# Optimization experiments

Measured on AMD Instinct MI355X. Metric: run time of the kernel, lower is better.

The kernel has to match this reference:

```python
import jax, jax.numpy as jnp
import numpy as np

N = 50000   # num_of_nodes (cfg.dataset.num_nodes)
C = 128     # in_channels; TopKPooling ratio = C/N -> k = C pooled nodes
E = 800000  # num edges


def setup_inputs() -> dict:
    key = jax.random.key(0)
    ks = jax.random.split(key, 8)
    std = 1.0 / np.sqrt(C)
    X = jax.random.normal(ks[0], (N, C), dtype=jnp.float32)
    edge_index = jax.random.randint(ks[1], (2, E), 0, N, dtype=jnp.int64)
    edge_weight = jax.random.uniform(ks[2], (E,), dtype=jnp.float32)
    p = jax.random.normal(ks[3], (C,), dtype=jnp.float32)                      # TopKPooling projection
    W_ih = jax.random.normal(ks[4], (3 * C, C), dtype=jnp.float32) * std       # GRU input weights [r|z|n]
    W_hh = jax.random.normal(ks[5], (3 * C, C), dtype=jnp.float32) * std       # GRU hidden weights
    b_ih = jnp.zeros((3 * C,), dtype=jnp.float32)
    b_hh = jnp.zeros((3 * C,), dtype=jnp.float32)
    W_conv = jax.random.uniform(ks[6], (C, C), dtype=jnp.float32, minval=-std, maxval=std)  # GCN lin weight
    b_conv = jnp.zeros((C,), dtype=jnp.float32)
    return {"X": X, "edge_weight": edge_weight, "p": p, "W_ih": W_ih, "W_hh": W_hh,
            "b_ih": b_ih, "b_hh": b_hh, "W_conv": W_conv, "b_conv": b_conv,
            "edge_index": edge_index}


def _forward(X, edge_weight, p, W_ih, W_hh, b_ih, b_hh, W_conv, b_conv, edge_index):
    # ---- TopKPooling: score = X.p/||p||, pick top k=C nodes, gate with tanh ----
    score = X @ p / jnp.linalg.norm(p)                       # [N]
    top_vals, top_idx = jax.lax.top_k(score, C)              # k = C (ratio = C/N)
    X_tilde = X[top_idx] * jnp.tanh(top_vals)[:, None]       # [C, C]
    X_tilde = jax.lax.stop_gradient(X_tilde)                 # .detach() in original

    # ---- GRU single step: input X_tilde (batch=C), hidden h0 = W_conv ----
    gi = X_tilde @ W_ih.T + b_ih                             # [C, 3C]
    gh = W_conv @ W_hh.T + b_hh                              # [C, 3C]
    gi_r, gi_z, gi_n = jnp.split(gi, 3, axis=-1)
    gh_r, gh_z, gh_n = jnp.split(gh, 3, axis=-1)
    r = jax.nn.sigmoid(gi_r + gh_r)
    z = jax.nn.sigmoid(gi_z + gh_z)
    n = jnp.tanh(gi_n + r * gh_n)
    W_new = (1.0 - z) * n + z * W_conv                       # evolved GCN weight [C, C]

    # ---- GCNConv with self-loops + symmetric normalization ----
    src, dst = edge_index[0], edge_index[1]
    loop = jnp.arange(N, dtype=src.dtype)
    src2 = jnp.concatenate([src, loop])
    dst2 = jnp.concatenate([dst, loop])
    w2 = jnp.concatenate([edge_weight, jnp.ones((N,), dtype=edge_weight.dtype)])
    deg = jax.ops.segment_sum(w2, dst2, num_segments=N)      # [N]
    dinv = jnp.where(deg > 0, jax.lax.rsqrt(deg), 0.0)
    norm = dinv[src2] * w2 * dinv[dst2]                      # [E+N]
    Xw = X @ W_new.T                                         # [N, C]
    msg = Xw[src2] * norm[:, None]                           # gather + scale, [E+N, C]
    out = jax.ops.segment_sum(msg, dst2, num_segments=N)     # scatter-add, [N, C]
    return out + b_conv


def reference(X, edge_weight, p, W_ih, W_hh, b_ih, b_hh, W_conv, b_conv, edge_index):
    return _forward(X, edge_weight, p, W_ih, W_hh, b_ih, b_hh, W_conv, b_conv, edge_index)
```

## Files before the change

kernel.cpp:

```cpp
#include <hip/hip_runtime.h>
#include <hip/hip_fp16.h>
#include <math.h>

#define C 128
#define HB 2048
#define NS 4096
#define SHB 192

typedef __attribute__((ext_vector_type(8))) short bf16x8;
typedef __attribute__((ext_vector_type(4))) float f32x4;

__device__ inline unsigned ord_f32(float f) {
    unsigned u = __float_as_uint(f);
    return u ^ ((u & 0x80000000u) ? 0xFFFFFFFFu : 0x80000000u);
}
__device__ inline float unord_f32(unsigned u) {
    return __uint_as_float(u ^ ((u & 0x80000000u) ? 0x80000000u : 0xFFFFFFFFu));
}
__device__ inline short f2bf(float f) {
    unsigned u = __float_as_uint(f);
    return (short)((u + 0x7FFFu + ((u >> 16) & 1u)) >> 16);
}
__device__ inline float bf2f(short s) {
    return __uint_as_float(((unsigned)(unsigned short)s) << 16);
}

__global__ __launch_bounds__(1024) void k_front(const float* __restrict__ X,
                                                const float* __restrict__ p,
                                                float* __restrict__ scores,
                                                int* __restrict__ hist,
                                                const int* __restrict__ ei,
                                                int* __restrict__ rh,
                                                int N, int E, int NBIN, int NBLKE) {
    int t = threadIdx.x;
    if (blockIdx.x < SHB) {
        __shared__ int lh[HB];
        for (int i = t; i < HB; i += 1024) lh[i] = 0;
        __syncthreads();
        int gw   = blockIdx.x * 16 + (t >> 6);
        int lane = t & 63;
        const float2* p2 = (const float2*)p;
        float2 pv2 = p2[lane];
        for (int r = gw; r < N; r += SHB * 16) {
            const float2* xr = (const float2*)(X + (size_t)r * C);
            float2 x2 = xr[lane];
            float a = x2.x * pv2.x + x2.y * pv2.y;
            #pragma unroll
            for (int o = 32; o; o >>= 1) a += __shfl_down(a, o);
            if (lane == 0) {
                scores[r] = a;
                atomicAdd(&lh[ord_f32(a) >> 21], 1);
            }
        }
        __syncthreads();
        for (int i = t; i < HB; i += 1024) {
            int v = lh[i];
            if (v) atomicAdd(&hist[i], v);
        }
    } else {
        __shared__ int bh[8][256];
        int cp = (t >> 7) & 7;
        for (int i = t; i < 8 * 256; i += 1024) ((int*)bh)[i] = 0;
        __syncthreads();
        int eb = blockIdx.x - SHB;
        int e = eb * 2048 + t * 2;
        if (e + 1 < E) {
            int2 d2 = *(const int2*)(ei + E + e);
            atomicAdd(&bh[cp][d2.x >> 8], 1);
            atomicAdd(&bh[cp][d2.y >> 8], 1);
        } else if (e < E) {
            atomicAdd(&bh[cp][ei[E + e] >> 8], 1);
        }
        __syncthreads();
        for (int i = t; i < NBIN; i += 1024) {
            int s = 0;
            #pragma unroll
            for (int c = 0; c < 8; c++) s += bh[c][i];
            rh[(size_t)i * NBLKE + eb] = s;
        }
    }
}

__global__ __launch_bounds__(512) void k_rscanA(int* __restrict__ rh, int* __restrict__ tot, int NBLKE) {
    __shared__ int sc[512];
    int t = threadIdx.x;
    int bin = blockIdx.x;
    int v = (t < NBLKE) ? rh[(size_t)bin * NBLKE + t] : 0;
    sc[t] = v;
    __syncthreads();
    for (int off = 1; off < 512; off <<= 1) {
        int u = (t >= off) ? sc[t - off] : 0;
        __syncthreads();
        sc[t] += u;
        __syncthreads();
    }
    if (t < NBLKE) rh[(size_t)bin * NBLKE + t] = sc[t] - v;
    if (t == 511) tot[bin] = sc[511];
}

__global__ __launch_bounds__(1024) void k_rscat(const int* __restrict__ ei, const float* __restrict__ ew,
                                                const int* __restrict__ rh, const int* __restrict__ tot,
                                                unsigned long long* __restrict__ sorted,
                                                int E, int NBIN, int NBLKE) {
    __shared__ int sc[256];
    __shared__ int cur[256];
    int t = threadIdx.x;
    int eb = blockIdx.x;
    int v = 0;
    if (t < 256) {
        v = (t < NBIN) ? tot[t] : 0;
        sc[t] = v;
    }
    __syncthreads();
    for (int off = 1; off < 256; off <<= 1) {
        int u = (t < 256 && t >= off) ? sc[t - off] : 0;
        __syncthreads();
        if (t < 256) sc[t] += u;
        __syncthreads();
    }
    if (t < NBIN) cur[t] = (sc[t] - v) + rh[(size_t)t * NBLKE + eb];
    __syncthreads();
    int e = eb * 2048 + t * 2;
    #pragma unroll
    for (int j = 0; j < 2; j++) {
        int ee = e + j;
        if (ee < E) {
            int s = ei[ee], d = ei[E + ee];
            float w = ew[ee];
            int pos = atomicAdd(&cur[d >> 8], 1);
            unsigned long long pk = ((unsigned long long)(unsigned)d << 48)
                                  | ((unsigned long long)(unsigned short)s << 32)
                                  |  (unsigned long long)__float_as_uint(w);
            sorted[pos] = pk;
        }
    }
}

__global__ __launch_bounds__(1024) void k_bin(const unsigned long long* __restrict__ sorted,
                                              const int* __restrict__ tot,
                                              int* __restrict__ offs, float* __restrict__ dinv,
                                              unsigned* __restrict__ epack,
                                              int N, int E, int NBIN) {
    __shared__ int cnt[256];
    __shared__ float wsum[256];
    __shared__ int sc[256];
    __shared__ int cur2[256];
    __shared__ int s_base[2];
    int t = threadIdx.x;
    int b = blockIdx.x;
    int v = 0;
    if (t < 256) {
        v = (t < NBIN) ? tot[t] : 0;
        sc[t] = v;
    }
    __syncthreads();
    for (int off = 1; off < 256; off <<= 1) {
        int u = (t < 256 && t >= off) ? sc[t - off] : 0;
        __syncthreads();
        if (t < 256) sc[t] += u;
        __syncthreads();
    }
    if (t == b) { s_base[0] = sc[t] - v; s_base[1] = sc[t]; }
    __syncthreads();
    int s0 = s_base[0], s1 = s_base[1];
    for (int i = t; i < 256; i += 1024) { cnt[i] = 0; wsum[i] = 0.f; }
    __syncthreads();
    for (int i = s0 + t; i < s1; i += 1024) {
        unsigned long long pk = sorted[i];
        int d8 = (int)(pk >> 48) & 255;
        float w = __uint_as_float((unsigned)(pk & 0xFFFFFFFFull));
        atomicAdd(&cnt[d8], 1);
        atomicAdd(&wsum[d8], w);
    }
    __syncthreads();
    int cv = (t < 256) ? cnt[t] : 0;
    if (t < 256) sc[t] = cv;
    __syncthreads();
    for (int off = 1; off < 256; off <<= 1) {
        int u = (t < 256 && t >= off) ? sc[t - off] : 0;
        __syncthreads();
        if (t < 256) sc[t] += u;
        __syncthreads();
    }
    if (t < 256) {
        int loff = sc[t] - cv;
        cur2[t] = s0 + loff;
        int node = b * 256 + t;
        if (node < N) {
            offs[node] = s0 + loff;
            dinv[node] = rsqrtf(1.0f + wsum[t]);
        }
    }
    if (b == NBIN - 1 && t == 0) offs[N] = E;
    __syncthreads();
    for (int i = s0 + t; i < s1; i += 1024) {
        unsigned long long pk = sorted[i];
        int d8 = (int)(pk >> 48) & 255;
        unsigned src = (unsigned)((pk >> 32) & 0xFFFFu);
        float w = __uint_as_float((unsigned)(pk & 0xFFFFFFFFull));
        int pos = atomicAdd(&cur2[d8], 1);
        __half hw = __float2half(w);
        epack[pos] = ((unsigned)*(unsigned short*)&hw << 16) | src;
    }
}

__global__ __launch_bounds__(256) void k_filter(const float* __restrict__ scores,
                                                const int* __restrict__ hist,
                                                int* __restrict__ nc,
                                                unsigned long long* __restrict__ cand, int N) {
    __shared__ int sc[256];
    __shared__ int sT;
    int t = threadIdx.x;
    int loc[8];
    int sum = 0;
    #pragma unroll
    for (int s = 0; s < 8; s++) {
        loc[s] = hist[HB - 1 - (t * 8 + s)];
        sum += loc[s];
    }
    sc[t] = sum;
    __syncthreads();
    for (int off = 1; off < 256; off <<= 1) {
        int v = (t >= off) ? sc[t - off] : 0;
        __syncthreads();
        sc[t] += v;
        __syncthreads();
    }
    int run = sc[t] - sum;
    #pragma unroll
    for (int s = 0; s < 8; s++) {
        int b = HB - 1 - (t * 8 + s);
        int nr = run + loc[s];
        if (run < C && nr >= C) sT = b;
        run = nr;
    }
    __syncthreads();
    int T = sT;
    int i = blockIdx.x * 256 + t;
    if (i < N) {
        unsigned u = ord_f32(scores[i]);
        if ((int)(u >> 21) >= T) {
            int pos = atomicAdd(nc, 1);
            if (pos < NS)
                cand[pos] = ((unsigned long long)u << 32) | (unsigned)(~(unsigned)i);
        }
    }
}

__global__ __launch_bounds__(1024) void k_sel(const unsigned long long* __restrict__ cand,
                                              const int* __restrict__ nc,
                                              const float* __restrict__ p,
                                              int* __restrict__ tidx, float* __restrict__ gate) {
    __shared__ unsigned long long sk[NS];
    __shared__ float red[16];
    __shared__ float s_pn;
    int t = threadIdx.x;
    int M = *nc; if (M > NS) M = NS;
    int S = 256; while (S < M) S <<= 1;
    for (int i = t; i < S; i += 1024) sk[i] = (i < M) ? cand[i] : 0ULL;
    float pv = 0.f;
    if (t < C) { float x = p[t]; pv = x * x; }
    #pragma unroll
    for (int o = 32; o; o >>= 1) pv += __shfl_down(pv, o);
    if ((t & 63) == 0) red[t >> 6] = pv;
    __syncthreads();
    if (t == 0) {
        float s = 0.f;
        for (int i = 0; i < 16; i++) s += red[i];
        s_pn = sqrtf(s);
    }
    for (int k = 2; k <= S; k <<= 1) {
        for (int j = k >> 1; j > 0; j >>= 1) {
            __syncthreads();
            for (int idx = t; idx < S; idx += 1024) {
                int l = idx ^ j;
                if (l > idx) {
                    unsigned long long a = sk[idx], b = sk[l];
                    bool desc = (idx & k) == 0;
                    if (desc ? (a < b) : (a > b)) { sk[idx] = b; sk[l] = a; }
                }
            }
        }
    }
    __syncthreads();
    if (t < C) {
        unsigned long long g = sk[t];
        tidx[t] = (int)(~(unsigned)(g & 0xFFFFFFFFull));
        gate[t] = tanhf(unord_f32((unsigned)(g >> 32)) / s_pn);
    }
}

__global__ __launch_bounds__(256) void k_gru(const float* __restrict__ X,
                                             const int* __restrict__ tidx,
                                             const float* __restrict__ gate,
                                             const float* __restrict__ Wc,
                                             const float* __restrict__ W_ih, const float* __restrict__ W_hh,
                                             const float* __restrict__ b_ih, const float* __restrict__ b_hh,
                                             float* __restrict__ wnewT) {
    int t = threadIdx.x;
    int i = t & 127;
    int j = blockIdx.x * 2 + (t >> 7);
    int src = tidx[i];
    float g = gate[i];
    const float4* xr   = (const float4*)(X + (size_t)src * C);
    const float4* hr   = (const float4*)(Wc + (size_t)i * C);
    const float4* wri  = (const float4*)(W_ih + (size_t)j * C);
    const float4* wzi  = (const float4*)(W_ih + (size_t)(C + j) * C);
    const float4* wni  = (const float4*)(W_ih + (size_t)(2 * C + j) * C);
    const float4* wrh  = (const float4*)(W_hh + (size_t)j * C);
    const float4* wzh  = (const float4*)(W_hh + (size_t)(C + j) * C);
    const float4* wnh  = (const float4*)(W_hh + (size_t)(2 * C + j) * C);
    float gir = 0, giz = 0, gin = 0, ghr = 0, ghz = 0, ghn = 0;
    #pragma unroll 8
    for (int k4 = 0; k4 < C / 4; k4++) {
        float4 x = xr[k4], h = hr[k4], a;
        a = wri[k4]; gir += x.x * a.x + x.y * a.y + x.z * a.z + x.w * a.w;
        a = wzi[k4]; giz += x.x * a.x + x.y * a.y + x.z * a.z + x.w * a.w;
        a = wni[k4]; gin += x.x * a.x + x.y * a.y + x.z * a.z + x.w * a.w;
        a = wrh[k4]; ghr += h.x * a.x + h.y * a.y + h.z * a.z + h.w * a.w;
        a = wzh[k4]; ghz += h.x * a.x + h.y * a.y + h.z * a.z + h.w * a.w;
        a = wnh[k4]; ghn += h.x * a.x + h.y * a.y + h.z * a.z + h.w * a.w;
    }
    gir = g * gir + b_ih[j];         ghr += b_hh[j];
    giz = g * giz + b_ih[C + j];     ghz += b_hh[C + j];
    gin = g * gin + b_ih[2 * C + j]; ghn += b_hh[2 * C + j];
    float r = 1.f / (1.f + expf(-(gir + ghr)));
    float z = 1.f / (1.f + expf(-(giz + ghz)));
    float n = tanhf(gin + r * ghn);
    float wn = (1.f - z) * n + z * Wc[(size_t)i * C + j];
    wnewT[(size_t)j * C + i] = wn;
}

__global__ __launch_bounds__(256) void k_xw(const float* __restrict__ X,
                                            const float* __restrict__ wnewT,
                                            const float* __restrict__ dinv,
                                            unsigned* __restrict__ xwh, int N) {
    __shared__ short Bh[C * C];
    __shared__ short Bl[C * C];
    int t = threadIdx.x;
    for (int idx = t; idx < C * C; idx += 256) {
        int k = idx >> 7, c = idx & 127;
        float wv = wnewT[idx];
        short hi = f2bf(wv);
        float lo = wv - bf2f(hi);
        int pos = c * C + (k ^ ((c & 15) << 3));
        Bh[pos] = hi;
        Bl[pos] = f2bf(lo);
    }
    __syncthreads();

    int wave = t >> 6, lane = t & 63;
    int ln = lane & 15, quad = lane >> 4;
    int r0 = blockIdx.x * 128 + wave * 32;

    f32x4 acc[2][8];
    #pragma unroll
    for (int mt = 0; mt < 2; mt++)
        #pragma unroll
        for (int ct = 0; ct < 8; ct++) { acc[mt][ct][0] = 0.f; acc[mt][ct][1] = 0.f; acc[mt][ct][2] = 0.f; acc[mt][ct][3] = 0.f; }

    int row0 = r0 + ln;       if (row0 >= N) row0 = N - 1;
    int row1 = r0 + 16 + ln;  if (row1 >= N) row1 = N - 1;
    const float* xr0 = X + (size_t)row0 * C + quad * 8;
    const float* xr1 = X + (size_t)row1 * C + quad * 8;

    for (int ks = 0; ks < 4; ks++) {
        float a0[8], a1[8];
        *(float4*)&a0[0] = *(const float4*)(xr0 + ks * 32);
        *(float4*)&a0[4] = *(const float4*)(xr0 + ks * 32 + 4);
        *(float4*)&a1[0] = *(const float4*)(xr1 + ks * 32);
        *(float4*)&a1[4] = *(const float4*)(xr1 + ks * 32 + 4);
        bf16x8 a0h, a0l, a1h, a1l;
        #pragma unroll
        for (int j = 0; j < 8; j++) {
            short h0 = f2bf(a0[j]); a0h[j] = h0; a0l[j] = f2bf(a0[j] - bf2f(h0));
            short h1 = f2bf(a1[j]); a1h[j] = h1; a1l[j] = f2bf(a1[j] - bf2f(h1));
        }
        int kb = ks * 32 + quad * 8;
        int koff = kb ^ (ln << 3);
        #pragma unroll
        for (int ct = 0; ct < 8; ct++) {
            int pos = (ct * 16 + ln) * C + koff;
            bf16x8 bh = *(bf16x8*)&Bh[pos];
            bf16x8 bl = *(bf16x8*)&Bl[pos];
            acc[0][ct] = __builtin_amdgcn_mfma_f32_16x16x32_bf16(a0h, bh, acc[0][ct], 0, 0, 0);
            acc[0][ct] = __builtin_amdgcn_mfma_f32_16x16x32_bf16(a0l, bh, acc[0][ct], 0, 0, 0);
            acc[0][ct] = __builtin_amdgcn_mfma_f32_16x16x32_bf16(a0h, bl, acc[0][ct], 0, 0, 0);
            acc[1][ct] = __builtin_amdgcn_mfma_f32_16x16x32_bf16(a1h, bh, acc[1][ct], 0, 0, 0);
            acc[1][ct] = __builtin_amdgcn_mfma_f32_16x16x32_bf16(a1l, bh, acc[1][ct], 0, 0, 0);
            acc[1][ct] = __builtin_amdgcn_mfma_f32_16x16x32_bf16(a1h, bl, acc[1][ct], 0, 0, 0);
        }
    }

    __half* H = (__half*)xwh;
    #pragma unroll
    for (int mt = 0; mt < 2; mt++) {
        int rbase = r0 + mt * 16 + quad * 4;
        #pragma unroll
        for (int reg = 0; reg < 4; reg++) {
            int r = rbase + reg;
            if (r < N) {
                float dvr = dinv[r];
                #pragma unroll
                for (int ct = 0; ct < 8; ct++) {
                    int col = ct * 16 + ln;
                    H[(size_t)r * C + col] = __float2half(acc[mt][ct][reg] * dvr);
                }
            }
        }
    }
}

__global__ __launch_bounds__(256) void k_gather(const unsigned* __restrict__ xwh,
                                                const int* __restrict__ offs,
                                                const unsigned* __restrict__ epack,
                                                const float* __restrict__ dinv,
                                                const float* __restrict__ b_conv,
                                                float* __restrict__ out, int N) {
    int t = threadIdx.x;
    int v = blockIdx.x * 4 + (t >> 6);
    int lane = t & 63;
    if (v >= N) return;
    float dv = dinv[v];
    unsigned uv = xwh[(size_t)v * 64 + lane];
    __half2 hv = *(__half2*)&uv;
    float acc0 = __low2float(hv);
    float acc1 = __high2float(hv);
    int e0 = offs[v], e1 = offs[v + 1];
    int e = e0;
    for (; e + 7 < e1; e += 8) {
        unsigned pk[8], ux[8];
        #pragma unroll
        for (int j = 0; j < 8; j++) pk[j] = __builtin_nontemporal_load(&epack[e + j]);
        #pragma unroll
        for (int j = 0; j < 8; j++) ux[j] = xwh[(size_t)(pk[j] & 0xFFFFu) * 64 + lane];
        #pragma unroll
        for (int j = 0; j < 8; j++) {
            unsigned short hs = (unsigned short)(pk[j] >> 16);
            float nm = __half2float(*(__half*)&hs);
            __half2 h = *(__half2*)&ux[j];
            acc0 += nm * __low2float(h);
            acc1 += nm * __high2float(h);
        }
    }
    for (; e + 3 < e1; e += 4) {
        unsigned pk[4], ux[4];
        #pragma unroll
        for (int j = 0; j < 4; j++) pk[j] = __builtin_nontemporal_load(&epack[e + j]);
        #pragma unroll
        for (int j = 0; j < 4; j++) ux[j] = xwh[(size_t)(pk[j] & 0xFFFFu) * 64 + lane];
        #pragma unroll
        for (int j = 0; j < 4; j++) {
            unsigned short hs = (unsigned short)(pk[j] >> 16);
            float nm = __half2float(*(__half*)&hs);
            __half2 h = *(__half2*)&ux[j];
            acc0 += nm * __low2float(h);
            acc1 += nm * __high2float(h);
        }
    }
    for (; e < e1; e++) {
        unsigned pA = __builtin_nontemporal_load(&epack[e]);
        unsigned uA = xwh[(size_t)(pA & 0xFFFFu) * 64 + lane];
        unsigned short hs = (unsigned short)(pA >> 16);
        float nA = __half2float(*(__half*)&hs);
        __half2 hA = *(__half2*)&uA;
        acc0 += nA * __low2float(hA);
        acc1 += nA * __high2float(hA);
    }
    const float2* b2 = (const float2*)b_conv;
    float2 bb = b2[lane];
    unsigned long long ov = ((unsigned long long)__float_as_uint(acc1 * dv + bb.y) << 32)
                          |  (unsigned long long)__float_as_uint(acc0 * dv + bb.x);
    __builtin_nontemporal_store(ov, (unsigned long long*)(out + (size_t)v * C) + lane);
}

extern "C" void kernel_launch(void* const* d_in, const int* in_sizes, int n_in,
                              void* d_out, int out_size, void* d_ws, size_t ws_size,
                              hipStream_t stream) {
    const float* X      = (const float*)d_in[0];
    const float* ew     = (const float*)d_in[1];
    const float* p      = (const float*)d_in[2];
    const float* W_ih   = (const float*)d_in[3];
    const float* W_hh   = (const float*)d_in[4];
    const float* b_ih   = (const float*)d_in[5];
    const float* b_hh   = (const float*)d_in[6];
    const float* W_conv = (const float*)d_in[7];
    const float* b_conv = (const float*)d_in[8];
    const int*   ei     = (const int*)d_in[9];
    const int N = in_sizes[0] / C;
    const int E = in_sizes[1];
    float* out = (float*)d_out;
    const int NB    = (N + 255) / 256;
    const int NBIN  = (N + 255) / 256;
    const int NBLKE = (E + 2047) / 2048;

    char* w = (char*)d_ws;
    auto alloc = [&](size_t bytes) -> void* {
        void* r = (void*)w;
        w += (bytes + 255) & ~(size_t)255;
        return r;
    };
    int*   hist   = (int*)alloc(HB * 4);
    int*   nc     = (int*)alloc(256);
    size_t zbytes = (size_t)(w - (char*)d_ws);
    float* scores = (float*)alloc((size_t)N * 4);
    float* dinv   = (float*)alloc((size_t)N * 4);
    int*   offs   = (int*)alloc((size_t)(N + 1) * 4);
    int*   rh     = (int*)alloc((size_t)NBIN * NBLKE * 4);
    int*   tot    = (int*)alloc((size_t)NBIN * 4);
    unsigned long long* cand = (unsigned long long*)alloc((size_t)NS * 8);
    int*   tidx   = (int*)alloc(C * 4);
    float* gate   = (float*)alloc(C * 4);
    float* wnewT  = (float*)alloc((size_t)C * C * 4);
    unsigned long long* sorted = (unsigned long long*)alloc((size_t)E * 8);
    unsigned* epack = (unsigned*)alloc((size_t)E * 4);
    unsigned* xwh = (unsigned*)alloc((size_t)N * 64 * 4);

    hipMemsetAsync(d_ws, 0, zbytes, stream);
    k_front<<<SHB + NBLKE, 1024, 0, stream>>>(X, p, scores, hist, ei, rh, N, E, NBIN, NBLKE);
    k_filter<<<NB, 256, 0, stream>>>(scores, hist, nc, cand, N);
    k_sel<<<1, 1024, 0, stream>>>(cand, nc, p, tidx, gate);
    k_gru<<<C / 2, 256, 0, stream>>>(X, tidx, gate, W_conv, W_ih, W_hh, b_ih, b_hh, wnewT);
    k_rscanA<<<NBIN, 512, 0, stream>>>(rh, tot, NBLKE);
    k_rscat<<<NBLKE, 1024, 0, stream>>>(ei, ew, rh, tot, sorted, E, NBIN, NBLKE);
    k_bin<<<NBIN, 1024, 0, stream>>>(sorted, tot, offs, dinv, epack, N, E, NBIN);
    k_xw<<<(N + 127) / 128, 256, 0, stream>>>(X, wnewT, dinv, xwh, N);
    k_gather<<<(N + 3) / 4, 256, 0, stream>>>(xwh, offs, epack, dinv, b_conv, out, N);
}
```

Before: 225.2 us.

## Fuse top-k filter and select, cache bin edges in LDS, unroll gather by 16

Merges the multi-block candidate filter and the single-block bitonic select into one single-block kernel that scans all scores and collects candidates in shared memory, removing a launch and the global candidate buffer and counter. k_bin now stashes its sorted edge slice in LDS during the counting pass so the second pass reads from LDS instead of global memory. The gather inner loop is unrolled from 8 to 16 edges for more loads in flight. The fused select runs the 50k-score scan on one block, which may be slower than the old parallel filter, and the larger LDS use in k_bin and the deeper unroll may cut occupancy.

```diff
diff --git a/kernel.cpp b/kernel.cpp
--- a/kernel.cpp
+++ b/kernel.cpp
@@ -6,6 +6,7 @@
 #define HB 2048
 #define NS 4096
 #define SHB 192
+#define BCAP 6144
 
 typedef __attribute__((ext_vector_type(8))) short bf16x8;
 typedef __attribute__((ext_vector_type(4))) float f32x4;
@@ -81,6 +82,78 @@
     }
 }
 
+__global__ __launch_bounds__(1024) void k_fsel(const float* __restrict__ scores,
+                                               const int* __restrict__ hist,
+                                               const float* __restrict__ p,
+                                               int* __restrict__ tidx, float* __restrict__ gate,
+                                               int N) {
+    __shared__ unsigned long long sk[NS];
+    __shared__ int hsc[1024];
+    __shared__ int sT;
+    __shared__ int s_nc;
+    __shared__ float red[16];
+    __shared__ float s_pn;
+    int t = threadIdx.x;
+    int b0 = HB - 1 - 2 * t, b1 = HB - 2 - 2 * t;
+    int l0 = hist[b0], l1 = hist[b1];
+    int sum = l0 + l1;
+    hsc[t] = sum;
+    if (t == 0) s_nc = 0;
+    __syncthreads();
+    for (int off = 1; off < 1024; off <<= 1) {
+        int v = (t >= off) ? hsc[t - off] : 0;
+        __syncthreads();
+        hsc[t] += v;
+        __syncthreads();
+    }
+    int run = hsc[t] - sum;
+    if (run < C && run + l0 >= C) sT = b0;
+    if (run + l0 < C && run + l0 + l1 >= C) sT = b1;
+    __syncthreads();
+    int T = sT;
+    for (int i = t; i < N; i += 1024) {
+        unsigned u = ord_f32(scores[i]);
+        if ((int)(u >> 21) >= T) {
+            int pos = atomicAdd(&s_nc, 1);
+            if (pos < NS)
+                sk[pos] = ((unsigned long long)u << 32) | (unsigned)(~(unsigned)i);
+        }
+    }
+    float pv = 0.f;
+    if (t < C) { float x = p[t]; pv = x * x; }
+    #pragma unroll
+    for (int o = 32; o; o >>= 1) pv += __shfl_down(pv, o);
+    if ((t & 63) == 0) red[t >> 6] = pv;
+    __syncthreads();
+    if (t == 0) {
+        float s = 0.f;
+        for (int i = 0; i < 16; i++) s += red[i];
+        s_pn = sqrtf(s);
+    }
+    int M = s_nc; if (M > NS) M = NS;
+    int S = 256; while (S < M) S <<= 1;
+    for (int i = t; i < S; i += 1024) if (i >= M) sk[i] = 0ULL;
+    for (int k = 2; k <= S; k <<= 1) {
+        for (int j = k >> 1; j > 0; j >>= 1) {
+            __syncthreads();
+            for (int idx = t; idx < S; idx += 1024) {
+                int l = idx ^ j;
+                if (l > idx) {
+                    unsigned long long a = sk[idx], b = sk[l];
+                    bool desc = (idx & k) == 0;
+                    if (desc ? (a < b) : (a > b)) { sk[idx] = b; sk[l] = a; }
+                }
+            }
+        }
+    }
+    __syncthreads();
+    if (t < C) {
+        unsigned long long g = sk[t];
+        tidx[t] = (int)(~(unsigned)(g & 0xFFFFFFFFull));
+        gate[t] = tanhf(unord_f32((unsigned)(g >> 32)) / s_pn);
+    }
+}
+
 __global__ __launch_bounds__(512) void k_rscanA(int* __restrict__ rh, int* __restrict__ tot, int NBLKE) {
     __shared__ int sc[512];
     int t = threadIdx.x;
@@ -141,6 +214,7 @@
                                               int* __restrict__ offs, float* __restrict__ dinv,
                                               unsigned* __restrict__ epack,
                                               int N, int E, int NBIN) {
+    __shared__ unsigned long long ebuf[BCAP];
     __shared__ int cnt[256];
     __shared__ float wsum[256];
     __shared__ int sc[256];
@@ -167,6 +241,8 @@
     __syncthreads();
     for (int i = s0 + t; i < s1; i += 1024) {
         unsigned long long pk = sorted[i];
+        int li = i - s0;
+        if (li < BCAP) ebuf[li] = pk;
         int d8 = (int)(pk >> 48) & 255;
         float w = __uint_as_float((unsigned)(pk & 0xFFFFFFFFull));
         atomicAdd(&cnt[d8], 1);
@@ -194,99 +270,14 @@
     if (b == NBIN - 1 && t == 0) offs[N] = E;
     __syncthreads();
     for (int i = s0 + t; i < s1; i += 1024) {
-        unsigned long long pk = sorted[i];
+        int li = i - s0;
+        unsigned long long pk = (li < BCAP) ? ebuf[li] : sorted[i];
         int d8 = (int)(pk >> 48) & 255;
         unsigned src = (unsigned)((pk >> 32) & 0xFFFFu);
         float w = __uint_as_float((unsigned)(pk & 0xFFFFFFFFull));
         int pos = atomicAdd(&cur2[d8], 1);
         __half hw = __float2half(w);
         epack[pos] = ((unsigned)*(unsigned short*)&hw << 16) | src;
-    }
-}
-
-__global__ __launch_bounds__(256) void k_filter(const float* __restrict__ scores,
-                                                const int* __restrict__ hist,
-                                                int* __restrict__ nc,
-                                                unsigned long long* __restrict__ cand, int N) {
-    __shared__ int sc[256];
-    __shared__ int sT;
-    int t = threadIdx.x;
-    int loc[8];
-    int sum = 0;
-    #pragma unroll
-    for (int s = 0; s < 8; s++) {
-        loc[s] = hist[HB - 1 - (t * 8 + s)];
-        sum += loc[s];
-    }
-    sc[t] = sum;
-    __syncthreads();
-    for (int off = 1; off < 256; off <<= 1) {
-        int v = (t >= off) ? sc[t - off] : 0;
-        __syncthreads();
-        sc[t] += v;
-        __syncthreads();
-    }
-    int run = sc[t] - sum;
-    #pragma unroll
-    for (int s = 0; s < 8; s++) {
-        int b = HB - 1 - (t * 8 + s);
-        int nr = run + loc[s];
-        if (run < C && nr >= C) sT = b;
-        run = nr;
-    }
-    __syncthreads();
-    int T = sT;
-    int i = blockIdx.x * 256 + t;
-    if (i < N) {
-        unsigned u = ord_f32(scores[i]);
-        if ((int)(u >> 21) >= T) {
-            int pos = atomicAdd(nc, 1);
-            if (pos < NS)
-                cand[pos] = ((unsigned long long)u << 32) | (unsigned)(~(unsigned)i);
-        }
-    }
-}
-
-__global__ __launch_bounds__(1024) void k_sel(const unsigned long long* __restrict__ cand,
-                                              const int* __restrict__ nc,
-                                              const float* __restrict__ p,
-                                              int* __restrict__ tidx, float* __restrict__ gate) {
-    __shared__ unsigned long long sk[NS];
-    __shared__ float red[16];
-    __shared__ float s_pn;
-    int t = threadIdx.x;
-    int M = *nc; if (M > NS) M = NS;
-    int S = 256; while (S < M) S <<= 1;
-    for (int i = t; i < S; i += 1024) sk[i] = (i < M) ? cand[i] : 0ULL;
-    float pv = 0.f;
-    if (t < C) { float x = p[t]; pv = x * x; }
-    #pragma unroll
-    for (int o = 32; o; o >>= 1) pv += __shfl_down(pv, o);
-    if ((t & 63) == 0) red[t >> 6] = pv;
-    __syncthreads();
-    if (t == 0) {
-        float s = 0.f;
-        for (int i = 0; i < 16; i++) s += red[i];
-        s_pn = sqrtf(s);
-    }
-    for (int k = 2; k <= S; k <<= 1) {
-        for (int j = k >> 1; j > 0; j >>= 1) {
-            __syncthreads();
-            for (int idx = t; idx < S; idx += 1024) {
-                int l = idx ^ j;
-                if (l > idx) {
-                    unsigned long long a = sk[idx], b = sk[l];
-                    bool desc = (idx & k) == 0;
-                    if (desc ? (a < b) : (a > b)) { sk[idx] = b; sk[l] = a; }
-                }
-            }
-        }
-    }
-    __syncthreads();
-    if (t < C) {
-        unsigned long long g = sk[t];
-        tidx[t] = (int)(~(unsigned)(g & 0xFFFFFFFFull));
-        gate[t] = tanhf(unord_f32((unsigned)(g >> 32)) / s_pn);
     }
 }
 
@@ -428,14 +419,14 @@
     float acc1 = __high2float(hv);
     int e0 = offs[v], e1 = offs[v + 1];
     int e = e0;
-    for (; e + 7 < e1; e += 8) {
-        unsigned pk[8], ux[8];
-        #pragma unroll
-        for (int j = 0; j < 8; j++) pk[j] = __builtin_nontemporal_load(&epack[e + j]);
-        #pragma unroll
-        for (int j = 0; j < 8; j++) ux[j] = xwh[(size_t)(pk[j] & 0xFFFFu) * 64 + lane];
-        #pragma unroll
-        for (int j = 0; j < 8; j++) {
+    for (; e + 15 < e1; e += 16) {
+        unsigned pk[16], ux[16];
+        #pragma unroll
+        for (int j = 0; j < 16; j++) pk[j] = __builtin_nontemporal_load(&epack[e + j]);
+        #pragma unroll
+        for (int j = 0; j < 16; j++) ux[j] = xwh[(size_t)(pk[j] & 0xFFFFu) * 64 + lane];
+        #pragma unroll
+        for (int j = 0; j < 16; j++) {
             unsigned short hs = (unsigned short)(pk[j] >> 16);
             float nm = __half2float(*(__half*)&hs);
             __half2 h = *(__half2*)&ux[j];
@@ -490,7 +481,6 @@
     const int N = in_sizes[0] / C;
     const int E = in_sizes[1];
     float* out = (float*)d_out;
-    const int NB    = (N + 255) / 256;
     const int NBIN  = (N + 255) / 256;
     const int NBLKE = (E + 2047) / 2048;
 
@@ -501,14 +491,12 @@
         return r;
     };
     int*   hist   = (int*)alloc(HB * 4);
-    int*   nc     = (int*)alloc(256);
     size_t zbytes = (size_t)(w - (char*)d_ws);
     float* scores = (float*)alloc((size_t)N * 4);
     float* dinv   = (float*)alloc((size_t)N * 4);
     int*   offs   = (int*)alloc((size_t)(N + 1) * 4);
     int*   rh     = (int*)alloc((size_t)NBIN * NBLKE * 4);
     int*   tot    = (int*)alloc((size_t)NBIN * 4);
-    unsigned long long* cand = (unsigned long long*)alloc((size_t)NS * 8);
     int*   tidx   = (int*)alloc(C * 4);
     float* gate   = (float*)alloc(C * 4);
     float* wnewT  = (float*)alloc((size_t)C * C * 4);
@@ -518,8 +506,7 @@
 
     hipMemsetAsync(d_ws, 0, zbytes, stream);
     k_front<<<SHB + NBLKE, 1024, 0, stream>>>(X, p, scores, hist, ei, rh, N, E, NBIN, NBLKE);
-    k_filter<<<NB, 256, 0, stream>>>(scores, hist, nc, cand, N);
-    k_sel<<<1, 1024, 0, stream>>>(cand, nc, p, tidx, gate);
+    k_fsel<<<1, 1024, 0, stream>>>(scores, hist, p, tidx, gate, N);
     k_gru<<<C / 2, 256, 0, stream>>>(X, tidx, gate, W_conv, W_ih, W_hh, b_ih, b_hh, wnewT);
     k_rscanA<<<NBIN, 512, 0, stream>>>(rh, tot, NBLKE);
     k_rscat<<<NBLKE, 1024, 0, stream>>>(ei, ew, rh, tot, sorted, E, NBIN, NBLKE);
```

Measured after the change: 237.4 us. +5.4%, slower.
